# Optimization experiments

Hardware: AMD Instinct MI355X
Metric: run time of the kernel (lower is better)

The kernel has to match this reference:

```python
import jax, jax.numpy as jnp
import numpy as np

_N = 512
_L = 65536


def setup_inputs() -> dict:
    key = jax.random.key(0)
    ks = jax.random.split(key, 11)
    N, L = _N, _L
    sc = 1.0 / np.sqrt(N)  # lecun-normal style scaling
    f = lambda k, s: jax.random.normal(k, s, dtype=jnp.float32)
    return {
        # stable DPLR spectrum: negative real parts
        "Lambda_re": -(jax.random.uniform(ks[0], (N,), dtype=jnp.float32) + 0.1),
        "Lambda_im": f(ks[1], (N,)),
        "p_re": f(ks[2], (N,)), "p_im": f(ks[3], (N,)),
        "q_re": f(ks[4], (N,)), "q_im": f(ks[5], (N,)),
        "Vc_re": f(ks[6], (N, N)) * sc, "Vc_im": f(ks[7], (N, N)) * sc,
        "Ct": f(ks[8], (1, N, 2)) * sc,
        "B": f(ks[9], (N, 1)) * sc,
        "log_step": jax.random.uniform(ks[10], (1,), dtype=jnp.float32)
                    * (np.log(0.1) - np.log(0.001)) + np.log(0.001),
        "L": L,
    }


def reference(Lambda_re, Lambda_im, p_re, p_im, q_re, q_im,
              Vc_re, Vc_im, Ct, B, log_step, L):
    Lambda = Lambda_re + 1j * Lambda_im            # (N,)
    p = p_re + 1j * p_im                           # (N,)
    q = q_re + 1j * q_im                           # (N,)
    Vc = Vc_re + 1j * Vc_im                        # (N,N)
    Ct_c = Ct[..., 0] + 1j * Ct[..., 1]            # (1,N)
    Bc = (Vc @ B.astype(Vc.dtype)).ravel()         # (N,) complex, B = Vc @ B
    step = jnp.exp(log_step)[0]

    # aterm = (Ct*, q*), bterm = (B, p)
    a0 = Ct_c.conj().ravel()
    a1 = q.conj()
    b0 = Bc
    b1 = p

    # roots of unity
    Omega = jnp.exp(-2j * jnp.pi * (jnp.arange(L) / L))   # (L,)
    g = (2.0 / step) * ((1.0 - Omega) / (1.0 + Omega))    # (L,) bilinear transform
    c = 2.0 / (1.0 + Omega)                               # (L,)

    # single fused Cauchy pass: resolvent (L,N) contracted with all 4 rank-1 terms
    r = 1.0 / (g[:, None] - Lambda[None, :])               # (L,N)
    terms = jnp.stack([a0 * b0, a0 * b1, a1 * b0, a1 * b1], axis=1)  # (N,4)
    K = r @ terms                                          # (L,4): k00,k01,k10,k11
    k00, k01, k10, k11 = K[:, 0], K[:, 1], K[:, 2], K[:, 3]

    atRoots = c * (k00 - k01 * (1.0 / (1.0 + k11)) * k10)  # Woodbury correction
    out = jnp.fft.ifft(atRoots, L).reshape(L)
    return out.real
```

## Files before the change

kernel.cpp:

```cpp
#include <hip/hip_runtime.h>
#include <math.h>

constexpr int WS_TERMS = 0;
constexpr int WS_ZT    = 8192;

__device__ __forceinline__ float sin2pi(float x) { return __builtin_amdgcn_sinf(x); }
__device__ __forceinline__ float cos2pi(float x) { return __builtin_amdgcn_cosf(x); }

__global__ __launch_bounds__(256) void k_setup(
    const float* __restrict__ Lr, const float* __restrict__ Li,
    const float* __restrict__ pr, const float* __restrict__ pi,
    const float* __restrict__ qr, const float* __restrict__ qi,
    const float* __restrict__ Vr, const float* __restrict__ Vi,
    const float* __restrict__ Ct, const float* __restrict__ Bv,
    const float* __restrict__ log_step,
    float* __restrict__ terms)
{
    __shared__ float red[8];
    int n = blockIdx.x;
    int t = threadIdx.x;
    float b0 = Bv[t], b1 = Bv[t + 256];
    float sr = fmaf(Vr[n*512 + t], b0, Vr[n*512 + t + 256] * b1);
    float si = fmaf(Vi[n*512 + t], b0, Vi[n*512 + t + 256] * b1);
    #pragma unroll
    for (int off = 32; off > 0; off >>= 1) {
        sr += __shfl_down(sr, off, 64);
        si += __shfl_down(si, off, 64);
    }
    if ((t & 63) == 0) { red[(t >> 6)*2] = sr; red[(t >> 6)*2 + 1] = si; }
    __syncthreads();
    if (t == 0) {
        float b0r = red[0] + red[2] + red[4] + red[6];
        float b0i = red[1] + red[3] + red[5] + red[7];
        double step = exp((double)log_step[0]);
        float t2s = (float)(2.0 / step);
        float lr  = Lr[n];
        float a0r = Ct[2*n], a0i = -Ct[2*n+1];
        float a1r = qr[n],   a1i = -qi[n];
        float b1r = pr[n],   b1i = pi[n];
        float* tm = terms + n * 12;
        tm[0]  = -lr;                 tm[1]  = Li[n];
        tm[2]  = a0r*b0r - a0i*b0i;   tm[3]  = a0r*b0i + a0i*b0r;
        tm[4]  = a0r*b1r - a0i*b1i;   tm[5]  = a0r*b1i + a0i*b1r;
        tm[6]  = a1r*b0r - a1i*b0i;   tm[7]  = a1r*b0i + a1i*b0r;
        tm[8]  = a1r*b1r - a1i*b1i;   tm[9]  = a1r*b1i + a1i*b1r;
        tm[10] = lr*lr;               tm[11] = t2s;
    }
}

__global__ __launch_bounds__(512) void k_mainA(
    const float* __restrict__ terms,
    float* __restrict__ ZTf)
{
    __shared__ float buf[9024];
    int tid = threadIdx.x;
    int l1  = blockIdx.x;

    {
        float4* dst = (float4*)buf;
        const float4* src = (const float4*)terms;
        #pragma unroll
        for (int i = 0; i < 3; ++i) dst[tid + 512*i] = src[tid + 512*i];
    }

    int u     = tid & 63;
    int chunk = tid >> 6;

    float t2s = terms[11];

    float T[4], g_i[4];
    #pragma unroll
    for (int q = 0; q < 4; ++q) {
        int l = l1 + 256*(u + 64*q);
        float tv2 = (float)l * (1.0f / 131072.0f);
        float sn  = sin2pi(tv2), cn = cos2pi(tv2);
        float Tq  = sn / cn;
        float gq  = t2s * Tq;
        if (!(fabsf(Tq) <= 1.0e6f)) { gq = 3e30f; Tq = 0.f; }
        T[q] = Tq; g_i[q] = gq;
    }
    __syncthreads();

    float ac[4][8];
    #pragma unroll
    for (int q = 0; q < 4; ++q)
        #pragma unroll
        for (int c = 0; c < 8; ++c) ac[q][c] = 0.f;

    const float4* t4 = (const float4*)buf + chunk * 64 * 3;
    #pragma unroll 2
    for (int n = 0; n < 64; ++n) {
        float4 Aq = t4[n*3 + 0];
        float4 Bq = t4[n*3 + 1];
        float4 Cq = t4[n*3 + 2];
        #pragma unroll
        for (int q = 0; q < 4; ++q) {
            float di = g_i[q] - Aq.y;
            float dd = fmaf(di, di, Cq.z);
            float iv = __builtin_amdgcn_rcpf(dd);
            float rr = Aq.x * iv;
            float ri = -di * iv;
            ac[q][0] = fmaf(rr, Aq.z, ac[q][0]); ac[q][0] = fmaf(-ri, Aq.w, ac[q][0]);
            ac[q][1] = fmaf(rr, Aq.w, ac[q][1]); ac[q][1] = fmaf( ri, Aq.z, ac[q][1]);
            ac[q][2] = fmaf(rr, Bq.x, ac[q][2]); ac[q][2] = fmaf(-ri, Bq.y, ac[q][2]);
            ac[q][3] = fmaf(rr, Bq.y, ac[q][3]); ac[q][3] = fmaf( ri, Bq.x, ac[q][3]);
            ac[q][4] = fmaf(rr, Bq.z, ac[q][4]); ac[q][4] = fmaf(-ri, Bq.w, ac[q][4]);
            ac[q][5] = fmaf(rr, Bq.w, ac[q][5]); ac[q][5] = fmaf( ri, Bq.z, ac[q][5]);
            ac[q][6] = fmaf(rr, Cq.x, ac[q][6]); ac[q][6] = fmaf(-ri, Cq.y, ac[q][6]);
            ac[q][7] = fmaf(rr, Cq.y, ac[q][7]); ac[q][7] = fmaf( ri, Cq.x, ac[q][7]);
        }
    }
    __syncthreads();

    float accR = 0.f, accI = 0.f;

    #pragma unroll
    for (int q = 0; q < 4; ++q) {
        if (chunk >= 4) {
            float* p = buf + 6144 + (chunk - 4) * 576 + u * 9;
            #pragma unroll
            for (int c = 0; c < 8; ++c) p[c] = ac[q][c];
        }
        __syncthreads();
        if (chunk < 4) {
            float* p = buf + 6144 + chunk * 576 + u * 9;
            #pragma unroll
            for (int c = 0; c < 8; ++c) p[c] += ac[q][c];
        }
        __syncthreads();

        {
            int a = (tid >> 3) * 9 + (tid & 7);
            buf[8448 + a] = buf[6144 + a] + buf[6720 + a] + buf[7296 + a] + buf[7872 + a];
        }
        __syncthreads();

        if (tid < 64) {
            const float* rd = buf + 8448 + tid * 9;
            float s0r = rd[0], s0i = rd[1], s1r = rd[2], s1i = rd[3];
            float s2r = rd[4], s2i = rd[5], s3r = rd[6], s3i = rd[7];
            float e1r = 1.f + s3r, e1i = s3i;
            float eiv = 1.0f / fmaf(e1r, e1r, e1i * e1i);
            float m_r = s1r * s2r - s1i * s2i;
            float m_i = s1r * s2i + s1i * s2r;
            float q_r = (m_r * e1r + m_i * e1i) * eiv;
            float q_i = (m_i * e1r - m_r * e1i) * eiv;
            float u_r = s0r - q_r;
            float u_i = s0i - q_i;
            float Tq  = T[q];
            ((float2*)buf)[tid] = make_float2(u_r - Tq * u_i, u_i + Tq * u_r);
        }
        __syncthreads();

        {
            int t1 = tid & 255;
            int s  = tid >> 8;
            int j0 = s * 32;
            int mm0 = ((q*64 + j0) * t1) & 255;
            float curR = cos2pi((float)mm0 * (1.0f/256.0f));
            float curI = sin2pi((float)mm0 * (1.0f/256.0f));
            float rotR = cos2pi((float)t1 * (1.0f/256.0f));
            float rotI = sin2pi((float)t1 * (1.0f/256.0f));
            const float2* xrow = (const float2*)buf;
            float yr = 0.f, yi = 0.f;
            #pragma unroll 8
            for (int j = j0; j < j0 + 32; ++j) {
                float2 x = xrow[j];
                yr = fmaf(x.x, curR, yr); yr = fmaf(-x.y, curI, yr);
                yi = fmaf(x.x, curI, yi); yi = fmaf( x.y, curR, yi);
                float nR = curR * rotR - curI * rotI;
                float nI = curR * rotI + curI * rotR;
                curR = nR; curI = nI;
            }
            ((float2*)(buf + 128))[tid] = make_float2(yr, yi);
        }
        __syncthreads();
        if (tid < 256) {
            const float2* pA = (const float2*)(buf + 128);
            float2 p0 = pA[tid], p1 = pA[tid + 256];
            accR += p0.x + p1.x;
            accI += p0.y + p1.y;
        }
    }

    if (tid < 256) {
        int mm = (l1 * tid) & 65535;
        float tv = (float)mm * (1.0f / 65536.0f);
        float twR = cos2pi(tv), twI = sin2pi(tv);
        ((float2*)ZTf)[tid * 256 + l1] =
            make_float2(accR * twR - accI * twI, accR * twI + accI * twR);
    }
}

__global__ __launch_bounds__(256) void k_fftB(
    const float* __restrict__ ZTf, float* __restrict__ out)
{
    __shared__ float buf2[768];
    int tid = threadIdx.x;
    int b   = blockIdx.x;
    int t1 = b >> 2;
    int qT = b & 3;
    {
        float2 v = ((const float2*)ZTf)[t1 * 256 + tid];
        ((float2*)buf2)[tid] = v;
    }
    int k2 = tid & 63;
    int s  = tid >> 6;
    int t2 = qT * 64 + k2;
    int m0 = (s * t2) & 3;
    float curR = (m0 == 0) ? 1.f : (m0 == 2 ? -1.f : 0.f);
    float curI = (m0 == 1) ? 1.f : (m0 == 3 ? -1.f : 0.f);
    float rotR = cos2pi((float)t2 * (1.0f / 256.0f));
    float rotI = sin2pi((float)t2 * (1.0f / 256.0f));
    __syncthreads();
    const float2* zrow = (const float2*)buf2;
    float o = 0.f;
    #pragma unroll 8
    for (int j = s * 64; j < s * 64 + 64; ++j) {
        float2 z = zrow[j];
        o = fmaf(z.x, curR, o);
        o = fmaf(-z.y, curI, o);
        float nR = curR * rotR - curI * rotI;
        float nI = curR * rotI + curI * rotR;
        curR = nR; curI = nI;
    }
    buf2[512 + tid] = o;
    __syncthreads();
    if (tid < 64) {
        float sum = buf2[512+tid] + buf2[512+tid+64] + buf2[512+tid+128] + buf2[512+tid+192];
        out[t1 + 256 * (qT * 64 + tid)] = sum * (1.0f / 65536.0f);
    }
}

extern "C" void kernel_launch(void* const* d_in, const int* in_sizes, int n_in,
                              void* d_out, int out_size, void* d_ws, size_t ws_size,
                              hipStream_t stream)
{
    const float* Lambda_re = (const float*)d_in[0];
    const float* Lambda_im = (const float*)d_in[1];
    const float* p_re      = (const float*)d_in[2];
    const float* p_im      = (const float*)d_in[3];
    const float* q_re      = (const float*)d_in[4];
    const float* q_im      = (const float*)d_in[5];
    const float* Vc_re     = (const float*)d_in[6];
    const float* Vc_im     = (const float*)d_in[7];
    const float* Ct        = (const float*)d_in[8];
    const float* Bv        = (const float*)d_in[9];
    const float* log_step  = (const float*)d_in[10];

    float* wsf   = (float*)d_ws;
    float* terms = wsf + WS_TERMS;
    float* ZT    = wsf + WS_ZT;
    float* outp  = (float*)d_out;

    k_setup<<<512, 256, 0, stream>>>(Lambda_re, Lambda_im, p_re, p_im, q_re, q_im,
                                     Vc_re, Vc_im, Ct, Bv, log_step, terms);
    k_mainA<<<256, 512, 0, stream>>>(terms, ZT);
    k_fftB<<<1024, 256, 0, stream>>>(ZT, outp);
}
```

Baseline: 108.1 us.

## Fuse setup, Cauchy and FFT kernels into one cooperative launch with grid syncs

Merges the three kernel launches into a single cooperative kernel of 256 blocks, separated by grid-wide barriers. Each block now handles two setup rows and, in the final phase, one full row of the second FFT pass instead of a quarter row. This removes two kernel launch gaps and inter-kernel drain, but adds grid.sync overhead and reduces parallelism in the final FFT stage from 1024 blocks to 256.

```diff
diff --git a/kernel.cpp b/kernel.cpp
--- a/kernel.cpp
+++ b/kernel.cpp
@@ -1,5 +1,8 @@
 #include <hip/hip_runtime.h>
+#include <hip/hip_cooperative_groups.h>
 #include <math.h>
+
+namespace cg = cooperative_groups;
 
 constexpr int WS_TERMS = 0;
 constexpr int WS_ZT    = 8192;
@@ -7,228 +10,232 @@
 __device__ __forceinline__ float sin2pi(float x) { return __builtin_amdgcn_sinf(x); }
 __device__ __forceinline__ float cos2pi(float x) { return __builtin_amdgcn_cosf(x); }
 
-__global__ __launch_bounds__(256) void k_setup(
+__global__ __launch_bounds__(512) void k_fused(
     const float* __restrict__ Lr, const float* __restrict__ Li,
     const float* __restrict__ pr, const float* __restrict__ pi,
     const float* __restrict__ qr, const float* __restrict__ qi,
     const float* __restrict__ Vr, const float* __restrict__ Vi,
     const float* __restrict__ Ct, const float* __restrict__ Bv,
     const float* __restrict__ log_step,
-    float* __restrict__ terms)
-{
-    __shared__ float red[8];
-    int n = blockIdx.x;
-    int t = threadIdx.x;
-    float b0 = Bv[t], b1 = Bv[t + 256];
-    float sr = fmaf(Vr[n*512 + t], b0, Vr[n*512 + t + 256] * b1);
-    float si = fmaf(Vi[n*512 + t], b0, Vi[n*512 + t + 256] * b1);
-    #pragma unroll
-    for (int off = 32; off > 0; off >>= 1) {
-        sr += __shfl_down(sr, off, 64);
-        si += __shfl_down(si, off, 64);
-    }
-    if ((t & 63) == 0) { red[(t >> 6)*2] = sr; red[(t >> 6)*2 + 1] = si; }
-    __syncthreads();
-    if (t == 0) {
-        float b0r = red[0] + red[2] + red[4] + red[6];
-        float b0i = red[1] + red[3] + red[5] + red[7];
-        double step = exp((double)log_step[0]);
-        float t2s = (float)(2.0 / step);
-        float lr  = Lr[n];
-        float a0r = Ct[2*n], a0i = -Ct[2*n+1];
-        float a1r = qr[n],   a1i = -qi[n];
-        float b1r = pr[n],   b1i = pi[n];
-        float* tm = terms + n * 12;
-        tm[0]  = -lr;                 tm[1]  = Li[n];
-        tm[2]  = a0r*b0r - a0i*b0i;   tm[3]  = a0r*b0i + a0i*b0r;
-        tm[4]  = a0r*b1r - a0i*b1i;   tm[5]  = a0r*b1i + a0i*b1r;
-        tm[6]  = a1r*b0r - a1i*b0i;   tm[7]  = a1r*b0i + a1i*b0r;
-        tm[8]  = a1r*b1r - a1i*b1i;   tm[9]  = a1r*b1i + a1i*b1r;
-        tm[10] = lr*lr;               tm[11] = t2s;
-    }
-}
-
-__global__ __launch_bounds__(512) void k_mainA(
-    const float* __restrict__ terms,
-    float* __restrict__ ZTf)
+    float* __restrict__ terms, float* __restrict__ ZTf, float* __restrict__ out)
 {
     __shared__ float buf[9024];
+    cg::grid_group grid = cg::this_grid();
     int tid = threadIdx.x;
-    int l1  = blockIdx.x;
+    int b   = blockIdx.x;
 
     {
-        float4* dst = (float4*)buf;
-        const float4* src = (const float4*)terms;
-        #pragma unroll
-        for (int i = 0; i < 3; ++i) dst[tid + 512*i] = src[tid + 512*i];
+        int half = tid >> 8;
+        int t    = tid & 255;
+        int n    = 2*b + half;
+        float b0 = Bv[t], b1 = Bv[t + 256];
+        float sr = fmaf(Vr[n*512 + t], b0, Vr[n*512 + t + 256] * b1);
+        float si = fmaf(Vi[n*512 + t], b0, Vi[n*512 + t + 256] * b1);
+        #pragma unroll
+        for (int off = 32; off > 0; off >>= 1) {
+            sr += __shfl_down(sr, off, 64);
+            si += __shfl_down(si, off, 64);
+        }
+        if ((t & 63) == 0) {
+            buf[half*8 + (t >> 6)*2]     = sr;
+            buf[half*8 + (t >> 6)*2 + 1] = si;
+        }
+        __syncthreads();
+        if (t == 0) {
+            const float* rd = buf + half*8;
+            float b0r = rd[0] + rd[2] + rd[4] + rd[6];
+            float b0i = rd[1] + rd[3] + rd[5] + rd[7];
+            double step = exp((double)log_step[0]);
+            float t2s = (float)(2.0 / step);
+            float lr  = Lr[n];
+            float a0r = Ct[2*n], a0i = -Ct[2*n+1];
+            float a1r = qr[n],   a1i = -qi[n];
+            float b1r = pr[n],   b1i = pi[n];
+            float* tm = terms + n * 12;
+            tm[0]  = -lr;                 tm[1]  = Li[n];
+            tm[2]  = a0r*b0r - a0i*b0i;   tm[3]  = a0r*b0i + a0i*b0r;
+            tm[4]  = a0r*b1r - a0i*b1i;   tm[5]  = a0r*b1i + a0i*b1r;
+            tm[6]  = a1r*b0r - a1i*b0i;   tm[7]  = a1r*b0i + a1i*b0r;
+            tm[8]  = a1r*b1r - a1i*b1i;   tm[9]  = a1r*b1i + a1i*b1r;
+            tm[10] = lr*lr;               tm[11] = t2s;
+        }
     }
-
-    int u     = tid & 63;
-    int chunk = tid >> 6;
-
-    float t2s = terms[11];
-
-    float T[4], g_i[4];
-    #pragma unroll
-    for (int q = 0; q < 4; ++q) {
-        int l = l1 + 256*(u + 64*q);
-        float tv2 = (float)l * (1.0f / 131072.0f);
-        float sn  = sin2pi(tv2), cn = cos2pi(tv2);
-        float Tq  = sn / cn;
-        float gq  = t2s * Tq;
-        if (!(fabsf(Tq) <= 1.0e6f)) { gq = 3e30f; Tq = 0.f; }
-        T[q] = Tq; g_i[q] = gq;
+    grid.sync();
+
+    {
+        int l1 = b;
+
+        {
+            float4* dst = (float4*)buf;
+            const float4* src = (const float4*)terms;
+            #pragma unroll
+            for (int i = 0; i < 3; ++i) dst[tid + 512*i] = src[tid + 512*i];
+        }
+
+        int u     = tid & 63;
+        int chunk = tid >> 6;
+
+        float t2s = terms[11];
+
+        float T[4], g_i[4];
+        #pragma unroll
+        for (int q = 0; q < 4; ++q) {
+            int l = l1 + 256*(u + 64*q);
+            float tv2 = (float)l * (1.0f / 131072.0f);
+            float sn  = sin2pi(tv2), cn = cos2pi(tv2);
+            float Tq  = sn / cn;
+            float gq  = t2s * Tq;
+            if (!(fabsf(Tq) <= 1.0e6f)) { gq = 3e30f; Tq = 0.f; }
+            T[q] = Tq; g_i[q] = gq;
+        }
+        __syncthreads();
+
+        float ac[4][8];
+        #pragma unroll
+        for (int q = 0; q < 4; ++q)
+            #pragma unroll
+            for (int c = 0; c < 8; ++c) ac[q][c] = 0.f;
+
+        const float4* t4 = (const float4*)buf + chunk * 64 * 3;
+        #pragma unroll 2
+        for (int n = 0; n < 64; ++n) {
+            float4 Aq = t4[n*3 + 0];
+            float4 Bq = t4[n*3 + 1];
+            float4 Cq = t4[n*3 + 2];
+            #pragma unroll
+            for (int q = 0; q < 4; ++q) {
+                float di = g_i[q] - Aq.y;
+                float dd = fmaf(di, di, Cq.z);
+                float iv = __builtin_amdgcn_rcpf(dd);
+                float rr = Aq.x * iv;
+                float ri = -di * iv;
+                ac[q][0] = fmaf(rr, Aq.z, ac[q][0]); ac[q][0] = fmaf(-ri, Aq.w, ac[q][0]);
+                ac[q][1] = fmaf(rr, Aq.w, ac[q][1]); ac[q][1] = fmaf( ri, Aq.z, ac[q][1]);
+                ac[q][2] = fmaf(rr, Bq.x, ac[q][2]); ac[q][2] = fmaf(-ri, Bq.y, ac[q][2]);
+                ac[q][3] = fmaf(rr, Bq.y, ac[q][3]); ac[q][3] = fmaf( ri, Bq.x, ac[q][3]);
+                ac[q][4] = fmaf(rr, Bq.z, ac[q][4]); ac[q][4] = fmaf(-ri, Bq.w, ac[q][4]);
+                ac[q][5] = fmaf(rr, Bq.w, ac[q][5]); ac[q][5] = fmaf( ri, Bq.z, ac[q][5]);
+                ac[q][6] = fmaf(rr, Cq.x, ac[q][6]); ac[q][6] = fmaf(-ri, Cq.y, ac[q][6]);
+                ac[q][7] = fmaf(rr, Cq.y, ac[q][7]); ac[q][7] = fmaf( ri, Cq.x, ac[q][7]);
+            }
+        }
+        __syncthreads();
+
+        float accR = 0.f, accI = 0.f;
+
+        #pragma unroll
+        for (int q = 0; q < 4; ++q) {
+            if (chunk >= 4) {
+                float* p = buf + 6144 + (chunk - 4) * 576 + u * 9;
+                #pragma unroll
+                for (int c = 0; c < 8; ++c) p[c] = ac[q][c];
+            }
+            __syncthreads();
+            if (chunk < 4) {
+                float* p = buf + 6144 + chunk * 576 + u * 9;
+                #pragma unroll
+                for (int c = 0; c < 8; ++c) p[c] += ac[q][c];
+            }
+            __syncthreads();
+
+            {
+                int a = (tid >> 3) * 9 + (tid & 7);
+                buf[8448 + a] = buf[6144 + a] + buf[6720 + a] + buf[7296 + a] + buf[7872 + a];
+            }
+            __syncthreads();
+
+            if (tid < 64) {
+                const float* rd = buf + 8448 + tid * 9;
+                float s0r = rd[0], s0i = rd[1], s1r = rd[2], s1i = rd[3];
+                float s2r = rd[4], s2i = rd[5], s3r = rd[6], s3i = rd[7];
+                float e1r = 1.f + s3r, e1i = s3i;
+                float eiv = 1.0f / fmaf(e1r, e1r, e1i * e1i);
+                float m_r = s1r * s2r - s1i * s2i;
+                float m_i = s1r * s2i + s1i * s2r;
+                float q_r = (m_r * e1r + m_i * e1i) * eiv;
+                float q_i = (m_i * e1r - m_r * e1i) * eiv;
+                float u_r = s0r - q_r;
+                float u_i = s0i - q_i;
+                float Tq  = T[q];
+                ((float2*)buf)[tid] = make_float2(u_r - Tq * u_i, u_i + Tq * u_r);
+            }
+            __syncthreads();
+
+            {
+                int t1 = tid & 255;
+                int s  = tid >> 8;
+                int j0 = s * 32;
+                int mm0 = ((q*64 + j0) * t1) & 255;
+                float curR = cos2pi((float)mm0 * (1.0f/256.0f));
+                float curI = sin2pi((float)mm0 * (1.0f/256.0f));
+                float rotR = cos2pi((float)t1 * (1.0f/256.0f));
+                float rotI = sin2pi((float)t1 * (1.0f/256.0f));
+                const float2* xrow = (const float2*)buf;
+                float yr = 0.f, yi = 0.f;
+                #pragma unroll 8
+                for (int j = j0; j < j0 + 32; ++j) {
+                    float2 x = xrow[j];
+                    yr = fmaf(x.x, curR, yr); yr = fmaf(-x.y, curI, yr);
+                    yi = fmaf(x.x, curI, yi); yi = fmaf( x.y, curR, yi);
+                    float nR = curR * rotR - curI * rotI;
+                    float nI = curR * rotI + curI * rotR;
+                    curR = nR; curI = nI;
+                }
+                ((float2*)(buf + 128))[tid] = make_float2(yr, yi);
+            }
+            __syncthreads();
+            if (tid < 256) {
+                const float2* pA = (const float2*)(buf + 128);
+                float2 p0 = pA[tid], p1 = pA[tid + 256];
+                accR += p0.x + p1.x;
+                accI += p0.y + p1.y;
+            }
+        }
+
+        if (tid < 256) {
+            int mm = (l1 * tid) & 65535;
+            float tv = (float)mm * (1.0f / 65536.0f);
+            float twR = cos2pi(tv), twI = sin2pi(tv);
+            ((float2*)ZTf)[tid * 256 + l1] =
+                make_float2(accR * twR - accI * twI, accR * twI + accI * twR);
+        }
     }
-    __syncthreads();
-
-    float ac[4][8];
-    #pragma unroll
-    for (int q = 0; q < 4; ++q)
-        #pragma unroll
-        for (int c = 0; c < 8; ++c) ac[q][c] = 0.f;
-
-    const float4* t4 = (const float4*)buf + chunk * 64 * 3;
-    #pragma unroll 2
-    for (int n = 0; n < 64; ++n) {
-        float4 Aq = t4[n*3 + 0];
-        float4 Bq = t4[n*3 + 1];
-        float4 Cq = t4[n*3 + 2];
-        #pragma unroll
-        for (int q = 0; q < 4; ++q) {
-            float di = g_i[q] - Aq.y;
-            float dd = fmaf(di, di, Cq.z);
-            float iv = __builtin_amdgcn_rcpf(dd);
-            float rr = Aq.x * iv;
-            float ri = -di * iv;
-            ac[q][0] = fmaf(rr, Aq.z, ac[q][0]); ac[q][0] = fmaf(-ri, Aq.w, ac[q][0]);
-            ac[q][1] = fmaf(rr, Aq.w, ac[q][1]); ac[q][1] = fmaf( ri, Aq.z, ac[q][1]);
-            ac[q][2] = fmaf(rr, Bq.x, ac[q][2]); ac[q][2] = fmaf(-ri, Bq.y, ac[q][2]);
-            ac[q][3] = fmaf(rr, Bq.y, ac[q][3]); ac[q][3] = fmaf( ri, Bq.x, ac[q][3]);
-            ac[q][4] = fmaf(rr, Bq.z, ac[q][4]); ac[q][4] = fmaf(-ri, Bq.w, ac[q][4]);
-            ac[q][5] = fmaf(rr, Bq.w, ac[q][5]); ac[q][5] = fmaf( ri, Bq.z, ac[q][5]);
-            ac[q][6] = fmaf(rr, Cq.x, ac[q][6]); ac[q][6] = fmaf(-ri, Cq.y, ac[q][6]);
-            ac[q][7] = fmaf(rr, Cq.y, ac[q][7]); ac[q][7] = fmaf( ri, Cq.x, ac[q][7]);
-        }
-    }
-    __syncthreads();
-
-    float accR = 0.f, accI = 0.f;
-
-    #pragma unroll
-    for (int q = 0; q < 4; ++q) {
-        if (chunk >= 4) {
-            float* p = buf + 6144 + (chunk - 4) * 576 + u * 9;
-            #pragma unroll
-            for (int c = 0; c < 8; ++c) p[c] = ac[q][c];
-        }
-        __syncthreads();
-        if (chunk < 4) {
-            float* p = buf + 6144 + chunk * 576 + u * 9;
-            #pragma unroll
-            for (int c = 0; c < 8; ++c) p[c] += ac[q][c];
-        }
-        __syncthreads();
-
-        {
-            int a = (tid >> 3) * 9 + (tid & 7);
-            buf[8448 + a] = buf[6144 + a] + buf[6720 + a] + buf[7296 + a] + buf[7872 + a];
-        }
-        __syncthreads();
-
-        if (tid < 64) {
-            const float* rd = buf + 8448 + tid * 9;
-            float s0r = rd[0], s0i = rd[1], s1r = rd[2], s1i = rd[3];
-            float s2r = rd[4], s2i = rd[5], s3r = rd[6], s3i = rd[7];
-            float e1r = 1.f + s3r, e1i = s3i;
-            float eiv = 1.0f / fmaf(e1r, e1r, e1i * e1i);
-            float m_r = s1r * s2r - s1i * s2i;
-            float m_i = s1r * s2i + s1i * s2r;
-            float q_r = (m_r * e1r + m_i * e1i) * eiv;
-            float q_i = (m_i * e1r - m_r * e1i) * eiv;
-            float u_r = s0r - q_r;
-            float u_i = s0i - q_i;
-            float Tq  = T[q];
-            ((float2*)buf)[tid] = make_float2(u_r - Tq * u_i, u_i + Tq * u_r);
-        }
-        __syncthreads();
-
-        {
-            int t1 = tid & 255;
-            int s  = tid >> 8;
-            int j0 = s * 32;
-            int mm0 = ((q*64 + j0) * t1) & 255;
-            float curR = cos2pi((float)mm0 * (1.0f/256.0f));
-            float curI = sin2pi((float)mm0 * (1.0f/256.0f));
-            float rotR = cos2pi((float)t1 * (1.0f/256.0f));
-            float rotI = sin2pi((float)t1 * (1.0f/256.0f));
-            const float2* xrow = (const float2*)buf;
-            float yr = 0.f, yi = 0.f;
+    grid.sync();
+
+    {
+        int t1 = b;
+        if (tid < 256)
+            ((float2*)buf)[tid] = ((const float2*)ZTf)[t1 * 256 + tid];
+        __syncthreads();
+        int tl = tid & 127;
+        int s  = tid >> 7;
+        const float2* zrow = (const float2*)buf;
+        #pragma unroll
+        for (int rep = 0; rep < 2; ++rep) {
+            int t2 = rep*128 + tl;
+            int m0 = (s * t2) & 3;
+            float curR = (m0 == 0) ? 1.f : (m0 == 2 ? -1.f : 0.f);
+            float curI = (m0 == 1) ? 1.f : (m0 == 3 ? -1.f : 0.f);
+            float rotR = cos2pi((float)t2 * (1.0f / 256.0f));
+            float rotI = sin2pi((float)t2 * (1.0f / 256.0f));
+            float o = 0.f;
             #pragma unroll 8
-            for (int j = j0; j < j0 + 32; ++j) {
-                float2 x = xrow[j];
-                yr = fmaf(x.x, curR, yr); yr = fmaf(-x.y, curI, yr);
-                yi = fmaf(x.x, curI, yi); yi = fmaf( x.y, curR, yi);
+            for (int j = s * 64; j < s * 64 + 64; ++j) {
+                float2 z = zrow[j];
+                o = fmaf(z.x, curR, o);
+                o = fmaf(-z.y, curI, o);
                 float nR = curR * rotR - curI * rotI;
                 float nI = curR * rotI + curI * rotR;
                 curR = nR; curI = nI;
             }
-            ((float2*)(buf + 128))[tid] = make_float2(yr, yi);
-        }
-        __syncthreads();
-        if (tid < 256) {
-            const float2* pA = (const float2*)(buf + 128);
-            float2 p0 = pA[tid], p1 = pA[tid + 256];
-            accR += p0.x + p1.x;
-            accI += p0.y + p1.y;
-        }
-    }
-
-    if (tid < 256) {
-        int mm = (l1 * tid) & 65535;
-        float tv = (float)mm * (1.0f / 65536.0f);
-        float twR = cos2pi(tv), twI = sin2pi(tv);
-        ((float2*)ZTf)[tid * 256 + l1] =
-            make_float2(accR * twR - accI * twI, accR * twI + accI * twR);
-    }
-}
-
-__global__ __launch_bounds__(256) void k_fftB(
-    const float* __restrict__ ZTf, float* __restrict__ out)
-{
-    __shared__ float buf2[768];
-    int tid = threadIdx.x;
-    int b   = blockIdx.x;
-    int t1 = b >> 2;
-    int qT = b & 3;
-    {
-        float2 v = ((const float2*)ZTf)[t1 * 256 + tid];
-        ((float2*)buf2)[tid] = v;
-    }
-    int k2 = tid & 63;
-    int s  = tid >> 6;
-    int t2 = qT * 64 + k2;
-    int m0 = (s * t2) & 3;
-    float curR = (m0 == 0) ? 1.f : (m0 == 2 ? -1.f : 0.f);
-    float curI = (m0 == 1) ? 1.f : (m0 == 3 ? -1.f : 0.f);
-    float rotR = cos2pi((float)t2 * (1.0f / 256.0f));
-    float rotI = sin2pi((float)t2 * (1.0f / 256.0f));
-    __syncthreads();
-    const float2* zrow = (const float2*)buf2;
-    float o = 0.f;
-    #pragma unroll 8
-    for (int j = s * 64; j < s * 64 + 64; ++j) {
-        float2 z = zrow[j];
-        o = fmaf(z.x, curR, o);
-        o = fmaf(-z.y, curI, o);
-        float nR = curR * rotR - curI * rotI;
-        float nI = curR * rotI + curI * rotR;
-        curR = nR; curI = nI;
-    }
-    buf2[512 + tid] = o;
-    __syncthreads();
-    if (tid < 64) {
-        float sum = buf2[512+tid] + buf2[512+tid+64] + buf2[512+tid+128] + buf2[512+tid+192];
-        out[t1 + 256 * (qT * 64 + tid)] = sum * (1.0f / 65536.0f);
+            buf[512 + s*128 + tl] = o;
+            __syncthreads();
+            if (tid < 128) {
+                float sum = buf[512+tid] + buf[640+tid] + buf[768+tid] + buf[896+tid];
+                out[t1 + 256 * t2] = sum * (1.0f / 65536.0f);
+            }
+            __syncthreads();
+        }
     }
 }
 
@@ -253,8 +260,12 @@
     float* ZT    = wsf + WS_ZT;
     float* outp  = (float*)d_out;
 
-    k_setup<<<512, 256, 0, stream>>>(Lambda_re, Lambda_im, p_re, p_im, q_re, q_im,
-                                     Vc_re, Vc_im, Ct, Bv, log_step, terms);
-    k_mainA<<<256, 512, 0, stream>>>(terms, ZT);
-    k_fftB<<<1024, 256, 0, stream>>>(ZT, outp);
+    void* args[] = {
+        (void*)&Lambda_re, (void*)&Lambda_im,
+        (void*)&p_re, (void*)&p_im, (void*)&q_re, (void*)&q_im,
+        (void*)&Vc_re, (void*)&Vc_im, (void*)&Ct, (void*)&Bv, (void*)&log_step,
+        (void*)&terms, (void*)&ZT, (void*)&outp
+    };
+    hipLaunchCooperativeKernel((const void*)k_fused, dim3(256), dim3(512),
+                               args, 0, stream);
 }
```

Measured after the change: 175.7 us. +62.4%, slower.

## Split Cauchy kernel across two blocks per column with packed-FP32 math

Applied to the files above, without the earlier changes.

The main Cauchy/FFT kernel now runs twice as many blocks, each handling half of the four frequency quarters. Each half writes its own partial ZT buffer, and the FFT kernel sums the two partials when loading. The inner resolvent loop uses 2-wide vector FMAs, which can map to packed FP32 instructions, and reads the terms directly from global memory instead of staging them in LDS, shrinking shared memory. The aim is better occupancy and less register pressure. The cost is an extra global buffer, and the duplicated per-block setup and DFT work is spread over more blocks.

```diff
diff --git a/kernel.cpp b/kernel.cpp
--- a/kernel.cpp
+++ b/kernel.cpp
@@ -1,5 +1,7 @@
 #include <hip/hip_runtime.h>
 #include <math.h>
+
+typedef float v2f __attribute__((ext_vector_type(2)));
 
 constexpr int WS_TERMS = 0;
 constexpr int WS_ZT    = 8192;
@@ -52,91 +54,103 @@
     const float* __restrict__ terms,
     float* __restrict__ ZTf)
 {
-    __shared__ float buf[9024];
+    __shared__ float buf[4160];
     int tid = threadIdx.x;
-    int l1  = blockIdx.x;
-
-    {
-        float4* dst = (float4*)buf;
-        const float4* src = (const float4*)terms;
-        #pragma unroll
-        for (int i = 0; i < 3; ++i) dst[tid + 512*i] = src[tid + 512*i];
-    }
+    int b   = blockIdx.x;
+    int l1  = b >> 1;
+    int h   = b & 1;
 
     int u     = tid & 63;
     int chunk = tid >> 6;
 
     float t2s = terms[11];
 
-    float T[4], g_i[4];
-    #pragma unroll
-    for (int q = 0; q < 4; ++q) {
-        int l = l1 + 256*(u + 64*q);
+    float T0, T1, g0, g1;
+    {
+        int l = l1 + 256*(h*128 + u);
         float tv2 = (float)l * (1.0f / 131072.0f);
-        float sn  = sin2pi(tv2), cn = cos2pi(tv2);
-        float Tq  = sn / cn;
-        float gq  = t2s * Tq;
+        float sn = sin2pi(tv2), cn = cos2pi(tv2);
+        float Tq = sn / cn;
+        float gq = t2s * Tq;
         if (!(fabsf(Tq) <= 1.0e6f)) { gq = 3e30f; Tq = 0.f; }
-        T[q] = Tq; g_i[q] = gq;
-    }
-    __syncthreads();
-
-    float ac[4][8];
-    #pragma unroll
-    for (int q = 0; q < 4; ++q)
-        #pragma unroll
-        for (int c = 0; c < 8; ++c) ac[q][c] = 0.f;
-
-    const float4* t4 = (const float4*)buf + chunk * 64 * 3;
-    #pragma unroll 2
+        T0 = Tq; g0 = gq;
+    }
+    {
+        int l = l1 + 256*(h*128 + 64 + u);
+        float tv2 = (float)l * (1.0f / 131072.0f);
+        float sn = sin2pi(tv2), cn = cos2pi(tv2);
+        float Tq = sn / cn;
+        float gq = t2s * Tq;
+        if (!(fabsf(Tq) <= 1.0e6f)) { gq = 3e30f; Tq = 0.f; }
+        T1 = Tq; g1 = gq;
+    }
+
+    v2f g2 = {g0, g1};
+    v2f acr0 = {0.f,0.f}, acr1 = {0.f,0.f}, acr2 = {0.f,0.f}, acr3 = {0.f,0.f};
+    v2f aci0 = {0.f,0.f}, aci1 = {0.f,0.f}, aci2 = {0.f,0.f}, aci3 = {0.f,0.f};
+
+    const float4* t4 = (const float4*)terms + chunk * 64 * 3;
+    #pragma unroll 4
     for (int n = 0; n < 64; ++n) {
         float4 Aq = t4[n*3 + 0];
         float4 Bq = t4[n*3 + 1];
         float4 Cq = t4[n*3 + 2];
-        #pragma unroll
-        for (int q = 0; q < 4; ++q) {
-            float di = g_i[q] - Aq.y;
-            float dd = fmaf(di, di, Cq.z);
-            float iv = __builtin_amdgcn_rcpf(dd);
-            float rr = Aq.x * iv;
-            float ri = -di * iv;
-            ac[q][0] = fmaf(rr, Aq.z, ac[q][0]); ac[q][0] = fmaf(-ri, Aq.w, ac[q][0]);
-            ac[q][1] = fmaf(rr, Aq.w, ac[q][1]); ac[q][1] = fmaf( ri, Aq.z, ac[q][1]);
-            ac[q][2] = fmaf(rr, Bq.x, ac[q][2]); ac[q][2] = fmaf(-ri, Bq.y, ac[q][2]);
-            ac[q][3] = fmaf(rr, Bq.y, ac[q][3]); ac[q][3] = fmaf( ri, Bq.x, ac[q][3]);
-            ac[q][4] = fmaf(rr, Bq.z, ac[q][4]); ac[q][4] = fmaf(-ri, Bq.w, ac[q][4]);
-            ac[q][5] = fmaf(rr, Bq.w, ac[q][5]); ac[q][5] = fmaf( ri, Bq.z, ac[q][5]);
-            ac[q][6] = fmaf(rr, Cq.x, ac[q][6]); ac[q][6] = fmaf(-ri, Cq.y, ac[q][6]);
-            ac[q][7] = fmaf(rr, Cq.y, ac[q][7]); ac[q][7] = fmaf( ri, Cq.x, ac[q][7]);
-        }
-    }
-    __syncthreads();
+        v2f di = g2 - (v2f){Aq.y, Aq.y};
+        v2f dd = __builtin_elementwise_fma(di, di, (v2f){Cq.z, Cq.z});
+        v2f iv = {__builtin_amdgcn_rcpf(dd.x), __builtin_amdgcn_rcpf(dd.y)};
+        v2f rr  = (v2f){Aq.x, Aq.x} * iv;
+        v2f mri = di * iv;
+        acr0 = __builtin_elementwise_fma(rr,   (v2f){Aq.z, Aq.z}, acr0);
+        acr0 = __builtin_elementwise_fma(mri,  (v2f){Aq.w, Aq.w}, acr0);
+        aci0 = __builtin_elementwise_fma(rr,   (v2f){Aq.w, Aq.w}, aci0);
+        aci0 = __builtin_elementwise_fma(-mri, (v2f){Aq.z, Aq.z}, aci0);
+        acr1 = __builtin_elementwise_fma(rr,   (v2f){Bq.x, Bq.x}, acr1);
+        acr1 = __builtin_elementwise_fma(mri,  (v2f){Bq.y, Bq.y}, acr1);
+        aci1 = __builtin_elementwise_fma(rr,   (v2f){Bq.y, Bq.y}, aci1);
+        aci1 = __builtin_elementwise_fma(-mri, (v2f){Bq.x, Bq.x}, aci1);
+        acr2 = __builtin_elementwise_fma(rr,   (v2f){Bq.z, Bq.z}, acr2);
+        acr2 = __builtin_elementwise_fma(mri,  (v2f){Bq.w, Bq.w}, acr2);
+        aci2 = __builtin_elementwise_fma(rr,   (v2f){Bq.w, Bq.w}, aci2);
+        aci2 = __builtin_elementwise_fma(-mri, (v2f){Bq.z, Bq.z}, aci2);
+        acr3 = __builtin_elementwise_fma(rr,   (v2f){Cq.x, Cq.x}, acr3);
+        acr3 = __builtin_elementwise_fma(mri,  (v2f){Cq.y, Cq.y}, acr3);
+        aci3 = __builtin_elementwise_fma(rr,   (v2f){Cq.y, Cq.y}, aci3);
+        aci3 = __builtin_elementwise_fma(-mri, (v2f){Cq.x, Cq.x}, aci3);
+    }
 
     float accR = 0.f, accI = 0.f;
 
     #pragma unroll
-    for (int q = 0; q < 4; ++q) {
+    for (int j = 0; j < 2; ++j) {
+        float av[8];
+        if (j == 0) {
+            av[0]=acr0.x; av[1]=aci0.x; av[2]=acr1.x; av[3]=aci1.x;
+            av[4]=acr2.x; av[5]=aci2.x; av[6]=acr3.x; av[7]=aci3.x;
+        } else {
+            av[0]=acr0.y; av[1]=aci0.y; av[2]=acr1.y; av[3]=aci1.y;
+            av[4]=acr2.y; av[5]=aci2.y; av[6]=acr3.y; av[7]=aci3.y;
+        }
         if (chunk >= 4) {
-            float* p = buf + 6144 + (chunk - 4) * 576 + u * 9;
+            float* p = buf + 1280 + (chunk - 4) * 576 + u * 9;
             #pragma unroll
-            for (int c = 0; c < 8; ++c) p[c] = ac[q][c];
+            for (int c = 0; c < 8; ++c) p[c] = av[c];
         }
         __syncthreads();
         if (chunk < 4) {
-            float* p = buf + 6144 + chunk * 576 + u * 9;
+            float* p = buf + 1280 + chunk * 576 + u * 9;
             #pragma unroll
-            for (int c = 0; c < 8; ++c) p[c] += ac[q][c];
+            for (int c = 0; c < 8; ++c) p[c] += av[c];
         }
         __syncthreads();
 
         {
             int a = (tid >> 3) * 9 + (tid & 7);
-            buf[8448 + a] = buf[6144 + a] + buf[6720 + a] + buf[7296 + a] + buf[7872 + a];
+            buf[3584 + a] = buf[1280 + a] + buf[1856 + a] + buf[2432 + a] + buf[3008 + a];
         }
         __syncthreads();
 
         if (tid < 64) {
-            const float* rd = buf + 8448 + tid * 9;
+            const float* rd = buf + 3584 + tid * 9;
             float s0r = rd[0], s0i = rd[1], s1r = rd[2], s1i = rd[3];
             float s2r = rd[4], s2i = rd[5], s3r = rd[6], s3i = rd[7];
             float e1r = 1.f + s3r, e1i = s3i;
@@ -147,7 +161,7 @@
             float q_i = (m_i * e1r - m_r * e1i) * eiv;
             float u_r = s0r - q_r;
             float u_i = s0i - q_i;
-            float Tq  = T[q];
+            float Tq  = (j == 0) ? T0 : T1;
             ((float2*)buf)[tid] = make_float2(u_r - Tq * u_i, u_i + Tq * u_r);
         }
         __syncthreads();
@@ -156,7 +170,8 @@
             int t1 = tid & 255;
             int s  = tid >> 8;
             int j0 = s * 32;
-            int mm0 = ((q*64 + j0) * t1) & 255;
+            int Q  = 2*h + j;
+            int mm0 = ((Q*64 + j0) * t1) & 255;
             float curR = cos2pi((float)mm0 * (1.0f/256.0f));
             float curI = sin2pi((float)mm0 * (1.0f/256.0f));
             float rotR = cos2pi((float)t1 * (1.0f/256.0f));
@@ -164,8 +179,8 @@
             const float2* xrow = (const float2*)buf;
             float yr = 0.f, yi = 0.f;
             #pragma unroll 8
-            for (int j = j0; j < j0 + 32; ++j) {
-                float2 x = xrow[j];
+            for (int jj = j0; jj < j0 + 32; ++jj) {
+                float2 x = xrow[jj];
                 yr = fmaf(x.x, curR, yr); yr = fmaf(-x.y, curI, yr);
                 yi = fmaf(x.x, curI, yi); yi = fmaf( x.y, curR, yi);
                 float nR = curR * rotR - curI * rotI;
@@ -187,7 +202,7 @@
         int mm = (l1 * tid) & 65535;
         float tv = (float)mm * (1.0f / 65536.0f);
         float twR = cos2pi(tv), twI = sin2pi(tv);
-        ((float2*)ZTf)[tid * 256 + l1] =
+        ((float2*)(ZTf + h * 131072))[tid * 256 + l1] =
             make_float2(accR * twR - accI * twI, accR * twI + accI * twR);
     }
 }
@@ -201,8 +216,13 @@
     int t1 = b >> 2;
     int qT = b & 3;
     {
-        float2 v = ((const float2*)ZTf)[t1 * 256 + tid];
-        ((float2*)buf2)[tid] = v;
+        float2 z = make_float2(0.f, 0.f);
+        #pragma unroll
+        for (int q = 0; q < 2; ++q) {
+            float2 v = ((const float2*)(ZTf + q * 131072))[t1 * 256 + tid];
+            z.x += v.x; z.y += v.y;
+        }
+        ((float2*)buf2)[tid] = z;
     }
     int k2 = tid & 63;
     int s  = tid >> 6;
@@ -255,6 +275,6 @@
 
     k_setup<<<512, 256, 0, stream>>>(Lambda_re, Lambda_im, p_re, p_im, q_re, q_im,
                                      Vc_re, Vc_im, Ct, Bv, log_step, terms);
-    k_mainA<<<256, 512, 0, stream>>>(terms, ZT);
+    k_mainA<<<512, 512, 0, stream>>>(terms, ZT);
     k_fftB<<<1024, 256, 0, stream>>>(ZT, outp);
 }
```

Result: slower. 112.7 us (+4.2%).
